# Optimization experiments

Measured on AMD Instinct MI355X. Metric: run time of the kernel, lower is better.

## Reference

```python
import jax, jax.numpy as jnp
import numpy as np
import math

B, S, D, H, HD, DC, FF, E, K = 4, 2048, 576, 9, 64, 64, 1536, 8, 2
EPS = 1e-6


def _rms(x):
    # RMSNorm with weight=ones (module instantiates a fresh RMSNorm in forward)
    return x / jnp.sqrt(jnp.mean(x * x, axis=-1, keepdims=True) + EPS)


def _expert(h, wa, wb, wc):
    return (jax.nn.gelu(h @ wa, approximate=False) * (h @ wc)) @ wb


def _forward(x, q_w, kv_w, o_w, gate_w, w1, w2, w3, sw1, sw2, sw3):
    # ---------------- MLA ----------------
    xn = _rms(x)
    q = (xn @ q_w).reshape(B, S, H, HD)
    kv = (xn @ kv_w).reshape(B, S, H, 2 * DC)
    k, v = kv[..., :DC], kv[..., DC:]
    # RoPE (complex-pair form) applied to q only, as in the source
    theta = 1.0 / (10000.0 ** (jnp.arange(0, HD, 2, dtype=jnp.float32) / HD))
    freqs = jnp.arange(S, dtype=jnp.float32)[:, None] * theta[None, :]  # [S, HD/2]
    cos = jnp.cos(freqs)[None, :, None, :]
    sin = jnp.sin(freqs)[None, :, None, :]
    qp = q.reshape(B, S, H, HD // 2, 2)
    qe, qo = qp[..., 0], qp[..., 1]
    q = jnp.stack([qe * cos - qo * sin, qe * sin + qo * cos], axis=-1).reshape(B, S, H, HD)
    # NOTE: source matmul attends head-vs-head per token: [B,S,H,HD] x [B,S,DC,H] -> [B,S,H,H]
    attn = jnp.einsum('bshd,bstd->bsht', q, k) / math.sqrt(HD)
    attn = jax.nn.softmax(attn, axis=-1)
    ao = jnp.einsum('bsht,bstd->bshd', attn, v)  # [B,S,H,DC]
    # faithful to torch: transpose(1,2).contiguous().view(B,S,D)
    ao = ao.transpose(0, 2, 1, 3).reshape(B, S, D)
    x = ao @ o_w + x
    # ---------------- MoE ----------------
    xn = _rms(x)
    gw = jax.nn.softmax(xn @ gate_w, axis=-1)  # [B,S,E]
    tw, ti = jax.lax.top_k(gw, K)
    tw = tw / jnp.sum(tw, axis=-1, keepdims=True)
    # combine weights per expert: zero for unselected experts (same math as masked loop)
    comb = jnp.sum(tw[..., None] * jax.nn.one_hot(ti, E, dtype=x.dtype), axis=-2)  # [B,S,E]
    h1 = jax.nn.gelu(jnp.einsum('bsd,edf->ebsf', xn, w1), approximate=False)
    h3 = jnp.einsum('bsd,edf->ebsf', xn, w3)
    eo = jnp.einsum('ebsf,efd->ebsd', h1 * h3, w2)  # [E,B,S,D]
    moe_out = jnp.einsum('ebsd,bse->bsd', eo, comb)
    shared = _expert(xn, sw1, sw2, sw3)
    return moe_out + shared + x


def setup_inputs() -> dict:
    key = jax.random.key(0)
    ks = jax.random.split(key, 11)
    s = 0.02
    return {
        'x': jax.random.normal(ks[0], (B, S, D), dtype=jnp.float32),
        'q_w': jax.random.normal(ks[1], (D, D), dtype=jnp.float32) * s,
        'kv_w': jax.random.normal(ks[2], (D, H * 2 * DC), dtype=jnp.float32) * s,
        'o_w': jax.random.normal(ks[3], (D, D), dtype=jnp.float32) * s,
        'gate_w': jax.random.normal(ks[4], (D, E), dtype=jnp.float32) * s,
        'w1': jax.random.normal(ks[5], (E, D, FF), dtype=jnp.float32) * s,
        'w2': jax.random.normal(ks[6], (E, FF, D), dtype=jnp.float32) * s,
        'w3': jax.random.normal(ks[7], (E, D, FF), dtype=jnp.float32) * s,
        'sw1': jax.random.normal(ks[8], (D, FF), dtype=jnp.float32) * s,
        'sw2': jax.random.normal(ks[9], (FF, D), dtype=jnp.float32) * s,
        'sw3': jax.random.normal(ks[10], (D, FF), dtype=jnp.float32) * s,
    }


def reference(x, q_w, kv_w, o_w, gate_w, w1, w2, w3, sw1, sw2, sw3):
    return _forward(x, q_w, kv_w, o_w, gate_w, w1, w2, w3, sw1, sw2, sw3)
```

## Files before the change

kernel.cpp:

```cpp
#include <hip/hip_runtime.h>
#include <math.h>

#define B_  4
#define S_  2048
#define D_  576
#define H_  9
#define HD_ 64
#define FF_ 1536
#define E_  8
#define TOK (B_*S_)
#define T1ROWS 17408

typedef unsigned int   u32x4  __attribute__((ext_vector_type(4)));
typedef unsigned short u16x8  __attribute__((ext_vector_type(8)));
typedef __bf16         bf16x8 __attribute__((ext_vector_type(8)));
typedef _Float16       f16x8  __attribute__((ext_vector_type(8)));
typedef float          f32x4  __attribute__((ext_vector_type(4)));

__device__ __forceinline__ float b2f(unsigned short u) {
    union { unsigned int i; float f; } v; v.i = ((unsigned int)u) << 16; return v.f;
}
__device__ __forceinline__ unsigned short f2b(float f) {
    unsigned int u = __builtin_bit_cast(unsigned int, f);
    unsigned int r = 0x7fffu + ((u >> 16) & 1u);
    return (unsigned short)((u + r) >> 16);
}

__global__ __launch_bounds__(256)
void rmsnorm_k(const float* __restrict__ x, unsigned short* __restrict__ xn) {
    int tok = blockIdx.x, tid = threadIdx.x;
    const float* xr = x + (size_t)tok * D_;
    float v0 = xr[tid];
    float v1 = xr[tid + 256];
    float v2 = (tid < D_ - 512) ? xr[tid + 512] : 0.f;
    float ss = v0*v0 + v1*v1 + v2*v2;
    #pragma unroll
    for (int d = 1; d < 64; d <<= 1) ss += __shfl_xor(ss, d, 64);
    __shared__ float red[4];
    if ((tid & 63) == 0) red[tid >> 6] = ss;
    __syncthreads();
    float tot = red[0] + red[1] + red[2] + red[3];
    float rms = rsqrtf(tot / (float)D_ + 1e-6f);
    unsigned short* orow = xn + (size_t)tok * D_;
    orow[tid]       = f2b(v0 * rms);
    orow[tid + 256] = f2b(v1 * rms);
    if (tid < D_ - 512) orow[tid + 512] = f2b(v2 * rms);
}

__global__ __launch_bounds__(256)
void rms32_k(const float* __restrict__ x, float* __restrict__ xn) {
    int tok = blockIdx.x, tid = threadIdx.x;
    const float* xr = x + (size_t)tok * D_;
    float v0 = xr[tid];
    float v1 = xr[tid + 256];
    float v2 = (tid < D_ - 512) ? xr[tid + 512] : 0.f;
    float ss = v0*v0 + v1*v1 + v2*v2;
    #pragma unroll
    for (int d = 1; d < 64; d <<= 1) ss += __shfl_xor(ss, d, 64);
    __shared__ float red[4];
    if ((tid & 63) == 0) red[tid >> 6] = ss;
    __syncthreads();
    float tot = red[0] + red[1] + red[2] + red[3];
    float rms = rsqrtf(tot / (float)D_ + 1e-6f);
    float* orow = xn + (size_t)tok * D_;
    orow[tid]       = v0 * rms;
    orow[tid + 256] = v1 * rms;
    if (tid < D_ - 512) orow[tid + 512] = v2 * rms;
}

__global__ __launch_bounds__(256)
void convw_k(const float* __restrict__ src, unsigned short* __restrict__ dst,
             int K, int N, long long sstr, long long dstr)
{
    __shared__ unsigned short t[64][72];
    int n0 = blockIdx.x * 64, k0 = blockIdx.y * 64;
    const float* s = src + (long long)blockIdx.z * sstr;
    unsigned short* d = dst + (long long)blockIdx.z * dstr;
    int tx = threadIdx.x & 63, ty = threadIdx.x >> 6;
    #pragma unroll
    for (int i = 0; i < 16; ++i) {
        int k = i * 4 + ty;
        t[k][tx] = f2b(s[(size_t)(k0 + k) * N + n0 + tx]);
    }
    __syncthreads();
    int r = threadIdx.x >> 3, c8 = (threadIdx.x & 7) * 8;
    #pragma unroll
    for (int it = 0; it < 2; ++it, r += 32) {
        u16x8 v;
        #pragma unroll
        for (int j = 0; j < 8; ++j) v[j] = t[c8 + j][r];
        *(u16x8*)&d[(size_t)(n0 + r) * K + k0 + c8] = v;
    }
}

__global__ __launch_bounds__(256)
void convS_k(const float* __restrict__ src,
             _Float16* __restrict__ dh, _Float16* __restrict__ dl,
             int K, int N)
{
    __shared__ _Float16 th[64][72], tl[64][72];
    int n0 = blockIdx.x * 64, k0 = blockIdx.y * 64;
    int tx = threadIdx.x & 63, ty = threadIdx.x >> 6;
    #pragma unroll
    for (int i = 0; i < 16; ++i) {
        int k = i * 4 + ty;
        float v = src[(size_t)(k0 + k) * N + n0 + tx];
        _Float16 h = (_Float16)v;
        th[k][tx] = h;
        tl[k][tx] = (_Float16)((v - (float)h) * 2048.0f);
    }
    __syncthreads();
    int r = threadIdx.x >> 3, c8 = (threadIdx.x & 7) * 8;
    #pragma unroll
    for (int it = 0; it < 2; ++it, r += 32) {
        f16x8 vh, vl;
        #pragma unroll
        for (int j = 0; j < 8; ++j) { vh[j] = th[c8 + j][r]; vl[j] = tl[c8 + j][r]; }
        *(f16x8*)&dh[(size_t)(n0 + r) * K + k0 + c8] = vh;
        *(f16x8*)&dl[(size_t)(n0 + r) * K + k0 + c8] = vl;
    }
}

template<int BN, int EPI, int WB>
__global__ __launch_bounds__(256)
void gemmS_k(const float* __restrict__ A, const float* __restrict__ Bm,
             const _Float16* __restrict__ Bhp, const _Float16* __restrict__ Blp,
             float* __restrict__ Cout, const float* __restrict__ resid,
             int M, int N, int K, int ldb)
{
    constexpr int BM = 128, BK = 64, LDT = BK + 8;
    constexpr int WM = BM / 2, WN = BN / 2, MI = WM / 16, NJ = WN / 16;
    __shared__ alignas(16) _Float16 Ah[BM][LDT], Al[BM][LDT];
    __shared__ alignas(16) _Float16 Bh[BN][LDT], Bl[BN][LDT];
    const int tid  = threadIdx.x;
    const int bn0  = blockIdx.x * BN, bm0 = blockIdx.y * BM;
    const int lane = tid & 63, wave = tid >> 6;
    const int l    = lane & 15, quad = lane >> 4;
    const int wm   = wave >> 1, wn = wave & 1;

    f32x4 accH[MI][NJ], accL[MI][NJ];
    #pragma unroll
    for (int mi = 0; mi < MI; ++mi)
        #pragma unroll
        for (int nj = 0; nj < NJ; ++nj) {
            accH[mi][nj] = (f32x4){0.f, 0.f, 0.f, 0.f};
            accL[mi][nj] = (f32x4){0.f, 0.f, 0.f, 0.f};
        }

    const int nK = K / BK;
    for (int kc = 0; kc < nK; ++kc) {
        __syncthreads();
        #pragma unroll
        for (int i = 0; i < (BM * BK) / 2048; ++i) {
            int u = i * 256 + tid;
            int r = u >> 3, c8 = (u & 7) * 8;
            const float* ga = A + (size_t)(bm0 + r) * K + kc * BK + c8;
            f16x8 hh, ll;
            #pragma unroll
            for (int j = 0; j < 8; ++j) {
                float v = ga[j];
                _Float16 h = (_Float16)v;
                hh[j] = h;
                ll[j] = (_Float16)((v - (float)h) * 2048.0f);
            }
            *(f16x8*)&Ah[r][c8] = hh;
            *(f16x8*)&Al[r][c8] = ll;
        }
        if constexpr (WB == 1) {
            #pragma unroll
            for (int i = 0; i < (BN * BK) / 2048; ++i) {
                int u = i * 256 + tid;
                int n = u >> 3, c8 = (u & 7) * 8;
                *(f16x8*)&Bh[n][c8] =
                    *(const f16x8*)(Bhp + (size_t)(bn0 + n) * K + kc * BK + c8);
                *(f16x8*)&Bl[n][c8] =
                    *(const f16x8*)(Blp + (size_t)(bn0 + n) * K + kc * BK + c8);
            }
        } else {
            #pragma unroll
            for (int i = 0; i < (BN * BK) / 2048; ++i) {
                int u = i * 256 + tid;
                int n = u % BN, k8 = (u / BN) * 8;
                const float* gB = Bm + (size_t)(kc * BK + k8) * ldb + bn0 + n;
                f16x8 hh, ll;
                #pragma unroll
                for (int j = 0; j < 8; ++j) {
                    float v = gB[(size_t)j * ldb];
                    _Float16 h = (_Float16)v;
                    hh[j] = h;
                    ll[j] = (_Float16)((v - (float)h) * 2048.0f);
                }
                *(f16x8*)&Bh[n][k8] = hh;
                *(f16x8*)&Bl[n][k8] = ll;
            }
        }
        __syncthreads();
        #pragma unroll
        for (int ks = 0; ks < BK; ks += 32) {
            f16x8 ah[MI], al[MI], bh[NJ], bl[NJ];
            #pragma unroll
            for (int mi = 0; mi < MI; ++mi) {
                ah[mi] = *(const f16x8*)&Ah[wm * WM + mi * 16 + l][ks + quad * 8];
                al[mi] = *(const f16x8*)&Al[wm * WM + mi * 16 + l][ks + quad * 8];
            }
            #pragma unroll
            for (int nj = 0; nj < NJ; ++nj) {
                bh[nj] = *(const f16x8*)&Bh[wn * WN + nj * 16 + l][ks + quad * 8];
                bl[nj] = *(const f16x8*)&Bl[wn * WN + nj * 16 + l][ks + quad * 8];
            }
            #pragma unroll
            for (int mi = 0; mi < MI; ++mi)
                #pragma unroll
                for (int nj = 0; nj < NJ; ++nj) {
                    accH[mi][nj] = __builtin_amdgcn_mfma_f32_16x16x32_f16(
                        ah[mi], bh[nj], accH[mi][nj], 0, 0, 0);
                    accL[mi][nj] = __builtin_amdgcn_mfma_f32_16x16x32_f16(
                        ah[mi], bl[nj], accL[mi][nj], 0, 0, 0);
                    accL[mi][nj] = __builtin_amdgcn_mfma_f32_16x16x32_f16(
                        al[mi], bh[nj], accL[mi][nj], 0, 0, 0);
                }
        }
    }
    #pragma unroll
    for (int mi = 0; mi < MI; ++mi)
        #pragma unroll
        for (int nj = 0; nj < NJ; ++nj)
            #pragma unroll
            for (int r = 0; r < 4; ++r) {
                int row = bm0 + wm * WM + mi * 16 + quad * 4 + r;
                int col = bn0 + wn * WN + nj * 16 + l;
                float v = accH[mi][nj][r] + accL[mi][nj][r] * (1.0f / 2048.0f);
                size_t idx = (size_t)row * N + col;
                if constexpr (EPI == 0) Cout[idx] = v;
                else                    Cout[idx] = v + resid[idx];
            }
}

template<int ROUTED>
__global__ __launch_bounds__(256, 2)
void gemm13_k(const unsigned short* __restrict__ A,
              const unsigned short* __restrict__ B1,
              const unsigned short* __restrict__ B3,
              unsigned short* __restrict__ T1o,
              const int* __restrict__ eidx,
              const int* __restrict__ counts,
              const int* __restrict__ offs,
              int M, int N, long long bstr)
{
    constexpr int BM = 128, BN = 128, BK = 64, LDT = BK + 8;
    constexpr int MI = 4, NJ = 4;
    __shared__ alignas(16) unsigned short As[BM][LDT];
    __shared__ alignas(16) unsigned short Bs1[BN][LDT];
    __shared__ alignas(16) unsigned short Bs3[BN][LDT];
    __shared__ int rowbuf[BM];
    const int tid  = threadIdx.x;
    const int bn0  = blockIdx.x * BN, bm0 = blockIdx.y * BM;
    const int lane = tid & 63, wave = tid >> 6;
    const int l    = lane & 15, quad = lane >> 4;
    const int wm   = wave >> 1, wn = wave & 1;
    const int rs   = tid >> 3, c8 = (tid & 7) * 8;

    int cnt = M, crow0 = 0;
    if constexpr (ROUTED) {
        int e = blockIdx.z;
        cnt = counts[e];
        if (bm0 >= cnt) return;
        crow0 = offs[e];
        B1 += (long long)e * bstr;
        B3 += (long long)e * bstr;
        if (tid < BM) {
            int rr = bm0 + tid;
            rowbuf[tid] = (rr < cnt) ? eidx[e * TOK + rr] : 0;
        }
        __syncthreads();
    }

    f32x4 acc1[MI][NJ], acc3[MI][NJ];
    #pragma unroll
    for (int mi = 0; mi < MI; ++mi)
        #pragma unroll
        for (int nj = 0; nj < NJ; ++nj) {
            acc1[mi][nj] = (f32x4){0.f, 0.f, 0.f, 0.f};
            acc3[mi][nj] = (f32x4){0.f, 0.f, 0.f, 0.f};
        }

    const int nK = D_ / BK;
    u32x4 ra[4], rb1[4], rb3[4];
    #pragma unroll
    for (int i = 0; i < 4; ++i) {
        int r = i * 32 + rs;
        int arow = ROUTED ? rowbuf[r] : (bm0 + r);
        ra[i]  = *(const u32x4*)(A  + (size_t)arow * D_ + c8);
        rb1[i] = *(const u32x4*)(B1 + (size_t)(bn0 + r) * D_ + c8);
        rb3[i] = *(const u32x4*)(B3 + (size_t)(bn0 + r) * D_ + c8);
    }
    for (int kc = 0; kc < nK; ++kc) {
        __syncthreads();
        #pragma unroll
        for (int i = 0; i < 4; ++i) {
            int r = i * 32 + rs;
            *(u32x4*)&As[r][c8]  = ra[i];
            *(u32x4*)&Bs1[r][c8] = rb1[i];
            *(u32x4*)&Bs3[r][c8] = rb3[i];
        }
        __syncthreads();
        if (kc + 1 < nK) {
            int ko = (kc + 1) * BK;
            #pragma unroll
            for (int i = 0; i < 4; ++i) {
                int r = i * 32 + rs;
                int arow = ROUTED ? rowbuf[r] : (bm0 + r);
                ra[i]  = *(const u32x4*)(A  + (size_t)arow * D_ + ko + c8);
                rb1[i] = *(const u32x4*)(B1 + (size_t)(bn0 + r) * D_ + ko + c8);
                rb3[i] = *(const u32x4*)(B3 + (size_t)(bn0 + r) * D_ + ko + c8);
            }
        }
        #pragma unroll
        for (int ks = 0; ks < BK; ks += 32) {
            bf16x8 af[MI], b1f[NJ], b3f[NJ];
            #pragma unroll
            for (int mi = 0; mi < MI; ++mi)
                af[mi] = __builtin_bit_cast(bf16x8,
                    *(const u32x4*)&As[wm * 64 + mi * 16 + l][ks + quad * 8]);
            #pragma unroll
            for (int nj = 0; nj < NJ; ++nj) {
                b1f[nj] = __builtin_bit_cast(bf16x8,
                    *(const u32x4*)&Bs1[wn * 64 + nj * 16 + l][ks + quad * 8]);
                b3f[nj] = __builtin_bit_cast(bf16x8,
                    *(const u32x4*)&Bs3[wn * 64 + nj * 16 + l][ks + quad * 8]);
            }
            #pragma unroll
            for (int mi = 0; mi < MI; ++mi)
                #pragma unroll
                for (int nj = 0; nj < NJ; ++nj) {
                    acc1[mi][nj] = __builtin_amdgcn_mfma_f32_16x16x32_bf16(
                        af[mi], b1f[nj], acc1[mi][nj], 0, 0, 0);
                    acc3[mi][nj] = __builtin_amdgcn_mfma_f32_16x16x32_bf16(
                        af[mi], b3f[nj], acc3[mi][nj], 0, 0, 0);
                }
        }
    }
    #pragma unroll
    for (int mi = 0; mi < MI; ++mi)
        #pragma unroll
        for (int nj = 0; nj < NJ; ++nj)
            #pragma unroll
            for (int r = 0; r < 4; ++r) {
                int lrow = bm0 + wm * 64 + mi * 16 + quad * 4 + r;
                int col  = bn0 + wn * 64 + nj * 16 + l;
                float hv = b2f(f2b(acc1[mi][nj][r]));
                float g  = 0.5f * hv * (1.0f + erff(hv * 0.70710678118654752f));
                T1o[(size_t)(crow0 + lrow) * N + col] = f2b(g * acc3[mi][nj][r]);
            }
}

template<int BN, int EPI, int ROUTED, int WB>
__global__ __launch_bounds__(256)
void gemm_k(const unsigned short* __restrict__ A,
            const void* __restrict__ Bm,
            void* __restrict__ Cout,
            const void* __restrict__ resid,
            const float* __restrict__ wgt,
            const int* __restrict__ eidx,
            const int* __restrict__ counts,
            const int* __restrict__ offs,
            int M, int N, int K, int ldb, long long bstr)
{
    constexpr int BM = 128, BK = 64, LDT = BK + 8;
    constexpr int WM = BM / 2, WN = BN / 2, MI = WM / 16, NJ = WN / 16;
    constexpr int AIT = (BM * BK) / 2048, BIT = (BN * BK) / 2048;
    __shared__ alignas(16) unsigned short As[BM][LDT];
    __shared__ alignas(16) unsigned short Bs[BN][LDT];
    __shared__ int rowbuf[BM];
    const int tid  = threadIdx.x;
    const int bn0  = blockIdx.x * BN, bm0 = blockIdx.y * BM;
    const int lane = tid & 63, wave = tid >> 6;
    const int l    = lane & 15, quad = lane >> 4;
    const int wm   = wave >> 1, wn = wave & 1;

    int cnt = M, crow0 = 0, ebase = 0;
    long long boff = 0;
    if constexpr (ROUTED) {
        int e = blockIdx.z;
        cnt = counts[e];
        if (bm0 >= cnt) return;
        crow0 = offs[e];
        ebase = e * TOK;
        boff  = (long long)e * bstr;
        if (tid < BM) {
            int rr = bm0 + tid;
            rowbuf[tid] = (rr < cnt) ? eidx[ebase + rr] : 0;
        }
        __syncthreads();
    }

    f32x4 acc[MI][NJ];
    #pragma unroll
    for (int mi = 0; mi < MI; ++mi)
        #pragma unroll
        for (int nj = 0; nj < NJ; ++nj) acc[mi][nj] = (f32x4){0.f, 0.f, 0.f, 0.f};

    const int nK = K / BK;
    u32x4 pa[AIT], pb[BIT];
    if constexpr (WB == 1) {
        const unsigned short* Bt = (const unsigned short*)Bm + boff;
        #pragma unroll
        for (int i = 0; i < AIT; ++i) {
            int r = i * 32 + (tid >> 3), c8 = (tid & 7) * 8;
            int arow;
            if constexpr (ROUTED && EPI != 5) arow = rowbuf[r];
            else if constexpr (ROUTED)        arow = crow0 + bm0 + r;
            else                              arow = bm0 + r;
            pa[i] = *(const u32x4*)(A + (size_t)arow * K + c8);
        }
        #pragma unroll
        for (int i = 0; i < BIT; ++i) {
            int n = i * 32 + (tid >> 3), c8 = (tid & 7) * 8;
            pb[i] = *(const u32x4*)(Bt + (size_t)(bn0 + n) * ldb + c8);
        }
    }
    for (int kc = 0; kc < nK; ++kc) {
        __syncthreads();
        if constexpr (WB == 1) {
            #pragma unroll
            for (int i = 0; i < AIT; ++i) {
                int r = i * 32 + (tid >> 3), c8 = (tid & 7) * 8;
                *(u32x4*)&As[r][c8] = pa[i];
            }
            #pragma unroll
            for (int i = 0; i < BIT; ++i) {
                int n = i * 32 + (tid >> 3), c8 = (tid & 7) * 8;
                *(u32x4*)&Bs[n][c8] = pb[i];
            }
        } else {
            #pragma unroll
            for (int i = 0; i < AIT; ++i) {
                int u = i * 256 + tid;
                int r = u >> 3, c8 = (u & 7) * 8;
                int arow;
                if constexpr (ROUTED && EPI != 5) arow = rowbuf[r];
                else if constexpr (ROUTED)        arow = crow0 + bm0 + r;
                else                              arow = bm0 + r;
                *(u32x4*)&As[r][c8] =
                    *(const u32x4*)(A + (size_t)arow * K + kc * BK + c8);
            }
            const float* Bf = (const float*)Bm + boff;
            #pragma unroll
            for (int i = 0; i < BIT; ++i) {
                int u = i * 256 + tid;
                int n = u % BN, k8 = (u / BN) * 8;
                const float* gB = Bf + (size_t)(kc * BK + k8) * ldb + bn0 + n;
                u16x8 tmp;
                #pragma unroll
                for (int j = 0; j < 8; ++j) tmp[j] = f2b(gB[(size_t)j * ldb]);
                *(u16x8*)&Bs[n][k8] = tmp;
            }
        }
        __syncthreads();
        if constexpr (WB == 1) {
            if (kc + 1 < nK) {
                int ko = (kc + 1) * BK;
                const unsigned short* Bt = (const unsigned short*)Bm + boff;
                #pragma unroll
                for (int i = 0; i < AIT; ++i) {
                    int r = i * 32 + (tid >> 3), c8 = (tid & 7) * 8;
                    int arow;
                    if constexpr (ROUTED && EPI != 5) arow = rowbuf[r];
                    else if constexpr (ROUTED)        arow = crow0 + bm0 + r;
                    else                              arow = bm0 + r;
                    pa[i] = *(const u32x4*)(A + (size_t)arow * K + ko + c8);
                }
                #pragma unroll
                for (int i = 0; i < BIT; ++i) {
                    int n = i * 32 + (tid >> 3), c8 = (tid & 7) * 8;
                    pb[i] = *(const u32x4*)(Bt + (size_t)(bn0 + n) * ldb + ko + c8);
                }
            }
        }
        #pragma unroll
        for (int ks = 0; ks < BK; ks += 32) {
            bf16x8 af[MI], bfr[NJ];
            #pragma unroll
            for (int mi = 0; mi < MI; ++mi)
                af[mi] = __builtin_bit_cast(bf16x8,
                    *(const u32x4*)&As[wm * WM + mi * 16 + l][ks + quad * 8]);
            #pragma unroll
            for (int nj = 0; nj < NJ; ++nj)
                bfr[nj] = __builtin_bit_cast(bf16x8,
                    *(const u32x4*)&Bs[wn * WN + nj * 16 + l][ks + quad * 8]);
            #pragma unroll
            for (int mi = 0; mi < MI; ++mi)
                #pragma unroll
                for (int nj = 0; nj < NJ; ++nj)
                    acc[mi][nj] = __builtin_amdgcn_mfma_f32_16x16x32_bf16(
                        af[mi], bfr[nj], acc[mi][nj], 0, 0, 0);
        }
    }
    #pragma unroll
    for (int mi = 0; mi < MI; ++mi)
        #pragma unroll
        for (int nj = 0; nj < NJ; ++nj)
            #pragma unroll
            for (int r = 0; r < 4; ++r) {
                int lrow = bm0 + wm * WM + mi * 16 + quad * 4 + r;
                int col  = bn0 + wn * WN + nj * 16 + l;
                float v = acc[mi][nj][r];
                if constexpr (EPI == 0) {
                    ((unsigned short*)Cout)[(size_t)(crow0 + lrow) * N + col] = f2b(v);
                } else if constexpr (EPI == 3) {
                    size_t ix = (size_t)(crow0 + lrow) * N + col;
                    float hv = b2f(((const unsigned short*)resid)[ix]);
                    float g = 0.5f * hv * (1.0f + erff(hv * 0.70710678118654752f));
                    ((unsigned short*)Cout)[ix] = f2b(g * v);
                } else if constexpr (EPI == 4) {
                    ((float*)Cout)[(size_t)lrow * N + col] += v;
                } else {
                    if (lrow < cnt) {
                        int   tok = rowbuf[lrow - bm0];
                        float sc  = wgt[ebase + lrow];
                        atomicAdd(&((float*)Cout)[(size_t)tok * N + col], sc * v);
                    }
                }
            }
}

__global__ __launch_bounds__(256)
void attn32_k(const float* __restrict__ q,
              const float* __restrict__ kv,
              float* __restrict__ ao,
              int pos0)
{
    int pl   = blockIdx.x * 4 + (threadIdx.x >> 6);
    int lane = threadIdx.x & 63;
    int pos  = pos0 + pl;
    int b = pos >> 11, s = pos & 2047;

    const float* qp  = q  + (size_t)pl * 576;
    const float* kvp = kv + (size_t)pl * 1152;

    int i = lane >> 1;
    float theta = powf(10000.f, -(float)i * (1.0f / 32.0f));
    float sn, cs;
    sincosf((float)s * theta, &sn, &cs);

    float qr[H_], kr[H_], vr[H_];
    #pragma unroll
    for (int h = 0; h < H_; ++h) {
        float qv = qp[h * 64 + lane];
        float qo = __shfl_xor(qv, 1, 64);
        qr[h] = (lane & 1) ? (qo * sn + qv * cs) : (qv * cs - qo * sn);
        kr[h] = kvp[h * 128 + lane];
        vr[h] = kvp[h * 128 + 64 + lane];
    }

    #pragma unroll
    for (int h = 0; h < H_; ++h) {
        float sc[H_];
        #pragma unroll
        for (int t = 0; t < H_; ++t) {
            float p = qr[h] * kr[t];
            #pragma unroll
            for (int d = 1; d < 64; d <<= 1) p += __shfl_xor(p, d, 64);
            sc[t] = p * 0.125f;
        }
        float mx = sc[0];
        #pragma unroll
        for (int t = 1; t < H_; ++t) mx = fmaxf(mx, sc[t]);
        float ssum = 0.f;
        #pragma unroll
        for (int t = 0; t < H_; ++t) { sc[t] = __expf(sc[t] - mx); ssum += sc[t]; }
        float inv = 1.0f / ssum;
        float ov = 0.f;
        #pragma unroll
        for (int t = 0; t < H_; ++t) ov += sc[t] * vr[t];
        ao[((size_t)(b * H_ + h) * S_ + s) * 64 + lane] = ov * inv;
    }
}

__global__ __launch_bounds__(256)
void gate1_k(const float* __restrict__ x2,
             const float* __restrict__ gw,
             float* __restrict__ tw,
             int*   __restrict__ tsel)
{
    int tok  = blockIdx.x * 4 + (threadIdx.x >> 6);
    int lane = threadIdx.x & 63;
    float acc[8];
    #pragma unroll
    for (int e = 0; e < 8; ++e) acc[e] = 0.f;
    float ss = 0.f;
    for (int d = lane; d < D_; d += 64) {
        float xv = x2[(size_t)tok * D_ + d];
        ss += xv * xv;
        const float* wr = gw + (size_t)d * 8;
        #pragma unroll
        for (int e = 0; e < 8; ++e) acc[e] += xv * wr[e];
    }
    #pragma unroll
    for (int d = 1; d < 64; d <<= 1) ss += __shfl_xor(ss, d, 64);
    #pragma unroll
    for (int e = 0; e < 8; ++e)
        #pragma unroll
        for (int d = 1; d < 64; d <<= 1) acc[e] += __shfl_xor(acc[e], d, 64);
    if (lane == 0) {
        float rms = rsqrtf(ss / (float)D_ + 1e-6f);
        #pragma unroll
        for (int e = 0; e < 8; ++e) acc[e] *= rms;
        float mx = acc[0];
        #pragma unroll
        for (int e = 1; e < 8; ++e) mx = fmaxf(mx, acc[e]);
        float g[8], ssum = 0.f;
        #pragma unroll
        for (int e = 0; e < 8; ++e) { g[e] = __expf(acc[e] - mx); ssum += g[e]; }
        #pragma unroll
        for (int e = 0; e < 8; ++e) g[e] /= ssum;
        int i1 = 0;
        #pragma unroll
        for (int e = 1; e < 8; ++e) if (g[e] > g[i1]) i1 = e;
        int i2 = -1;
        #pragma unroll
        for (int e = 0; e < 8; ++e)
            if (e != i1 && (i2 < 0 || g[e] > g[i2])) i2 = e;
        float s2 = g[i1] + g[i2];
        tw[(size_t)tok * 2 + 0] = g[i1] / s2;
        tw[(size_t)tok * 2 + 1] = g[i2] / s2;
        tsel[tok] = i1 | (i2 << 8);
    }
}

__global__ __launch_bounds__(256)
void gate2_k(const int*   __restrict__ tsel,
             const float* __restrict__ tw,
             float* __restrict__ wgt,
             int*   __restrict__ eidx,
             int*   __restrict__ counts)
{
    int e    = blockIdx.x;
    int tid  = threadIdx.x;
    int lane = tid & 63, wv = tid >> 6;
    __shared__ int wtot[4];
    int base = 0;
    for (int t0 = 0; t0 < TOK; t0 += 256) {
        int tok = t0 + tid;
        int s = tsel[tok];
        int hit = 0; float w = 0.f;
        if ((s & 255) == e)      { hit = 1; w = tw[(size_t)tok * 2 + 0]; }
        else if ((s >> 8) == e)  { hit = 1; w = tw[(size_t)tok * 2 + 1]; }
        unsigned long long m = __ballot(hit);
        int pre = __popcll(m & ((1ull << lane) - 1ull));
        if (lane == 0) wtot[wv] = __popcll(m);
        __syncthreads();
        int off = base;
        for (int q = 0; q < wv; ++q) off += wtot[q];
        if (hit) {
            int p = off + pre;
            eidx[e * TOK + p] = tok;
            wgt [e * TOK + p] = w;
        }
        base += wtot[0] + wtot[1] + wtot[2] + wtot[3];
        __syncthreads();
    }
    if (tid == 0) counts[e] = base;
}

__global__ void offs_k(const int* __restrict__ counts, int* __restrict__ offs) {
    if (threadIdx.x == 0) {
        int run = 0;
        for (int e = 0; e < 8; ++e) {
            offs[e] = run;
            run += ((counts[e] + 127) >> 7) << 7;
        }
    }
}

extern "C" void kernel_launch(void* const* d_in, const int* in_sizes, int n_in,
                              void* d_out, int out_size, void* d_ws, size_t ws_size,
                              hipStream_t stream)
{
    const float* x      = (const float*)d_in[0];
    const float* q_w    = (const float*)d_in[1];
    const float* kv_w   = (const float*)d_in[2];
    const float* o_w    = (const float*)d_in[3];
    const float* gate_w = (const float*)d_in[4];
    const float* w1     = (const float*)d_in[5];
    const float* w2     = (const float*)d_in[6];
    const float* w3     = (const float*)d_in[7];
    const float* sw1    = (const float*)d_in[8];
    const float* sw2    = (const float*)d_in[9];
    const float* sw3    = (const float*)d_in[10];
    float* out = (float*)d_out;

    const size_t XN = (size_t)TOK * D_ * 2;
    char* ws = (char*)d_ws;
    unsigned short* xn16 = (unsigned short*)ws;
    float*          ao32 = (float*)(ws + XN);

    const size_t QE = (size_t)D_ * D_, KVE = (size_t)1152 * D_;
    const size_t SW = (2 * QE + KVE) * 2 * 2;
    _Float16* qwh  = (_Float16*)(ws + 3 * XN);
    _Float16* qwl  = qwh  + QE;
    _Float16* kvwh = qwl  + QE;
    _Float16* kvwl = kvwh + KVE;
    _Float16* owh  = kvwl + KVE;
    _Float16* owl  = owh  + QE;

    bool convA = true;
    int TC = -1;
    for (int pass = 0; pass < 2; ++pass) {
        size_t base = 3 * XN + (convA ? SW : 0);
        if      (base + 8*XN    <= ws_size) { TC = 1; break; }
        else if (base + 8*XN/2  <= ws_size) { TC = 2; break; }
        else if (base + 8*XN/4  <= ws_size) { TC = 4; break; }
        else if (base + 8*XN/8  <= ws_size) { TC = 8; break; }
        else if (base + 8*XN/16 <= ws_size) { TC = 16; break; }
        else if (base + 8*XN/32 <= ws_size) { TC = 32; break; }
        else if (base + 8*XN/64 <= ws_size) { TC = 64; break; }
        convA = false;
    }
    if (TC < 0) { convA = false; TC = 64; }
    const int CT = TOK / TC;
    float* xn32c = (float*)(ws + 3*XN + (convA ? SW : 0));
    float* qc    = xn32c + (size_t)CT * D_;
    float* kvc   = qc    + (size_t)CT * D_;

    int*   counts = (int*)(ws + XN);
    int*   offs   = counts + 16;
    float* wgt    = (float*)(ws + XN + 256);
    int*   eidx   = (int*)  (ws + XN + 256 + (size_t)8 * TOK * 4);
    float* tw     = (float*)(ws + XN + 256 + (size_t)8 * TOK * 8);
    int*   tsel   = (int*)  (ws + XN + 256 + (size_t)8 * TOK * 8 + (size_t)TOK * 8);
    const size_t fixedG = XN + 256 + (size_t)8 * TOK * 8 + (size_t)TOK * 12;

    const size_t WELEM = (size_t)D_ * FF_;
    const size_t WSZ   = 27 * WELEM * 2;
    const size_t t1sz  = (size_t)T1ROWS * FF_ * 2;

    bool conv; int FC;
    if      (fixedG + WSZ + t1sz   <= ws_size) { conv = true;  FC = 1; }
    else if (fixedG + WSZ + t1sz/2 <= ws_size) { conv = true;  FC = 2; }
    else if (fixedG + WSZ + t1sz/4 <= ws_size) { conv = true;  FC = 4; }
    else if (fixedG + t1sz         <= ws_size) { conv = false; FC = 1; }
    else if (fixedG + t1sz/2       <= ws_size) { conv = false; FC = 2; }
    else                                       { conv = false; FC = 4; }
    const int FFc = FF_ / FC;

    unsigned short* wt1  = (unsigned short*)(ws + fixedG);
    unsigned short* wt3  = wt1 + 8 * WELEM;
    unsigned short* wt2  = wt3 + 8 * WELEM;
    unsigned short* swt1 = wt2 + 8 * WELEM;
    unsigned short* swt3 = swt1 + WELEM;
    unsigned short* swt2 = swt3 + WELEM;
    unsigned short* t1   = (unsigned short*)(ws + fixedG + (conv ? WSZ : 0));

    if (convA) {
        convS_k<<<dim3(D_/64,  D_/64), 256, 0, stream>>>(q_w,  qwh,  qwl,  D_, D_);
        convS_k<<<dim3(1152/64, D_/64), 256, 0, stream>>>(kv_w, kvwh, kvwl, D_, 1152);
        convS_k<<<dim3(D_/64,  D_/64), 256, 0, stream>>>(o_w,  owh,  owl,  D_, D_);
    }
    for (int t = 0; t < TC; ++t) {
        const float* xc = x + (size_t)t * CT * D_;
        rms32_k<<<CT, 256, 0, stream>>>(xc, xn32c);
        if (convA) {
            gemmS_k<64, 0, 1><<<dim3(D_ / 64, CT / 128), 256, 0, stream>>>(
                xn32c, nullptr, qwh, qwl, qc, nullptr, CT, D_, D_, D_);
            gemmS_k<64, 0, 1><<<dim3(1152 / 64, CT / 128), 256, 0, stream>>>(
                xn32c, nullptr, kvwh, kvwl, kvc, nullptr, CT, 1152, D_, D_);
        } else {
            gemmS_k<64, 0, 0><<<dim3(D_ / 64, CT / 128), 256, 0, stream>>>(
                xn32c, q_w, nullptr, nullptr, qc, nullptr, CT, D_, D_, D_);
            gemmS_k<64, 0, 0><<<dim3(1152 / 64, CT / 128), 256, 0, stream>>>(
                xn32c, kv_w, nullptr, nullptr, kvc, nullptr, CT, 1152, D_, 1152);
        }
        attn32_k<<<CT / 4, 256, 0, stream>>>(qc, kvc, ao32, t * CT);
    }
    if (convA)
        gemmS_k<64, 1, 1><<<dim3(D_ / 64, TOK / 128), 256, 0, stream>>>(
            ao32, nullptr, owh, owl, out, x, TOK, D_, D_, D_);
    else
        gemmS_k<64, 1, 0><<<dim3(D_ / 64, TOK / 128), 256, 0, stream>>>(
            ao32, o_w, nullptr, nullptr, out, x, TOK, D_, D_, D_);
    rmsnorm_k<<<TOK, 256, 0, stream>>>(out, xn16);
    gate1_k<<<TOK / 4, 256, 0, stream>>>(out, gate_w, tw, tsel);
    gate2_k<<<E_, 256, 0, stream>>>(tsel, tw, wgt, eidx, counts);
    offs_k<<<1, 64, 0, stream>>>(counts, offs);
    if (conv) {
        convw_k<<<dim3(FF_/64, D_/64, 8), 256, 0, stream>>>(
            w1, wt1, D_, FF_, (long long)D_ * FF_, (long long)FF_ * D_);
        convw_k<<<dim3(FF_/64, D_/64, 8), 256, 0, stream>>>(
            w3, wt3, D_, FF_, (long long)D_ * FF_, (long long)FF_ * D_);
        convw_k<<<dim3(D_/64, FF_/64, 8), 256, 0, stream>>>(
            w2, wt2, FF_, D_, (long long)FF_ * D_, (long long)D_ * FF_);
        convw_k<<<dim3(FF_/64, D_/64, 1), 256, 0, stream>>>(
            sw1, swt1, D_, FF_, 0, 0);
        convw_k<<<dim3(FF_/64, D_/64, 1), 256, 0, stream>>>(
            sw3, swt3, D_, FF_, 0, 0);
        convw_k<<<dim3(D_/64, FF_/64, 1), 256, 0, stream>>>(
            sw2, swt2, FF_, D_, 0, 0);
    }
    for (int c = 0; c < FC; ++c) {
        if (conv) {
            gemm13_k<1><<<dim3(FFc / 128, TOK / 128, E_), 256, 0, stream>>>(
                xn16, wt1 + (size_t)c * FFc * D_, wt3 + (size_t)c * FFc * D_,
                t1, eidx, counts, offs, TOK, FFc, (long long)FF_ * D_);
            gemm_k<192, 5, 1, 1><<<dim3(D_ / 192, TOK / 128, E_), 256, 0, stream>>>(
                t1, wt2 + (size_t)c * FFc, out, nullptr, wgt, eidx, counts, offs,
                TOK, D_, FFc, FF_, (long long)D_ * FF_);
            gemm13_k<0><<<dim3(FFc / 128, TOK / 128), 256, 0, stream>>>(
                xn16, swt1 + (size_t)c * FFc * D_, swt3 + (size_t)c * FFc * D_,
                t1, nullptr, nullptr, nullptr, TOK, FFc, 0);
            gemm_k<192, 4, 0, 1><<<dim3(D_ / 192, TOK / 128), 256, 0, stream>>>(
                t1, swt2 + (size_t)c * FFc, out, nullptr, nullptr, nullptr, nullptr, nullptr,
                TOK, D_, FFc, FF_, 0);
        } else {
            const float* w1c = w1 + (size_t)c * FFc;
            const float* w3c = w3 + (size_t)c * FFc;
            const float* w2c = w2 + (size_t)c * FFc * D_;
            gemm_k<128, 0, 1, 0><<<dim3(FFc / 128, TOK / 128, E_), 256, 0, stream>>>(
                xn16, w1c, t1, nullptr, wgt, eidx, counts, offs,
                TOK, FFc, D_, FF_, (long long)D_ * FF_);
            gemm_k<128, 3, 1, 0><<<dim3(FFc / 128, TOK / 128, E_), 256, 0, stream>>>(
                xn16, w3c, t1, t1, wgt, eidx, counts, offs,
                TOK, FFc, D_, FF_, (long long)D_ * FF_);
            gemm_k<64, 5, 1, 0><<<dim3(D_ / 64, TOK / 128, E_), 256, 0, stream>>>(
                t1, w2c, out, nullptr, wgt, eidx, counts, offs,
                TOK, D_, FFc, D_, (long long)FF_ * D_);
            gemm_k<128, 0, 0, 0><<<dim3(FFc / 128, TOK / 128), 256, 0, stream>>>(
                xn16, sw1 + (size_t)c * FFc, t1, nullptr, nullptr, nullptr, nullptr, nullptr,
                TOK, FFc, D_, FF_, 0);
            gemm_k<128, 3, 0, 0><<<dim3(FFc / 128, TOK / 128), 256, 0, stream>>>(
                xn16, sw3 + (size_t)c * FFc, t1, t1, nullptr, nullptr, nullptr, nullptr,
                TOK, FFc, D_, FF_, 0);
            gemm_k<64, 4, 0, 0><<<dim3(D_ / 64, TOK / 128), 256, 0, stream>>>(
                t1, sw2 + (size_t)c * FFc * D_, out, nullptr, nullptr, nullptr, nullptr, nullptr,
                TOK, D_, FFc, D_, 0);
        }
    }
}
```

Baseline: 704.1 us.

## Fold shared expert into routed MoE grid, swizzle LDS, merge weight conversions

The shared expert becomes a ninth 'expert' that every token routes to with weight one. Its up and down GEMMs then run inside the same routed launches as the eight experts, so two separate launches go away and the tail wave fills better. Weight conversion is merged into two launches, and the LDS tiles in the split-fp16 and bf16 GEMMs switch from padded rows to an XOR swizzle, which saves shared memory. gemm13 launch bounds rise to three blocks per SM to raise occupancy, at the cost of fewer registers per thread, and the t1 buffer grows to hold the extra rows.

```diff
diff --git a/kernel.cpp b/kernel.cpp
--- a/kernel.cpp
+++ b/kernel.cpp
@@ -10,6 +10,7 @@
 #define E_  8
 #define TOK (B_*S_)
 #define T1ROWS 17408
+#define T1ALL  25600
 
 typedef unsigned int   u32x4  __attribute__((ext_vector_type(4)));
 typedef unsigned short u16x8  __attribute__((ext_vector_type(8)));
@@ -69,13 +70,48 @@
 }
 
 __global__ __launch_bounds__(256)
-void convw_k(const float* __restrict__ src, unsigned short* __restrict__ dst,
-             int K, int N, long long sstr, long long dstr)
-{
+void convw13_k(const float* __restrict__ w1, const float* __restrict__ w3,
+               const float* __restrict__ sw1, const float* __restrict__ sw3,
+               unsigned short* __restrict__ wt1, unsigned short* __restrict__ wt3)
+{
+    const size_t WE = (size_t)D_ * FF_;
+    int z = blockIdx.z;
+    const float* s; unsigned short* d;
+    if (z < 8)       { s = w1 + (size_t)z * WE;       d = wt1 + (size_t)z * WE; }
+    else if (z == 8) { s = sw1;                        d = wt1 + 8 * WE; }
+    else if (z < 17) { s = w3 + (size_t)(z - 9) * WE;  d = wt3 + (size_t)(z - 9) * WE; }
+    else             { s = sw3;                        d = wt3 + 8 * WE; }
+    const int K = D_, N = FF_;
     __shared__ unsigned short t[64][72];
     int n0 = blockIdx.x * 64, k0 = blockIdx.y * 64;
-    const float* s = src + (long long)blockIdx.z * sstr;
-    unsigned short* d = dst + (long long)blockIdx.z * dstr;
+    int tx = threadIdx.x & 63, ty = threadIdx.x >> 6;
+    #pragma unroll
+    for (int i = 0; i < 16; ++i) {
+        int k = i * 4 + ty;
+        t[k][tx] = f2b(s[(size_t)(k0 + k) * N + n0 + tx]);
+    }
+    __syncthreads();
+    int r = threadIdx.x >> 3, c8 = (threadIdx.x & 7) * 8;
+    #pragma unroll
+    for (int it = 0; it < 2; ++it, r += 32) {
+        u16x8 v;
+        #pragma unroll
+        for (int j = 0; j < 8; ++j) v[j] = t[c8 + j][r];
+        *(u16x8*)&d[(size_t)(n0 + r) * K + k0 + c8] = v;
+    }
+}
+
+__global__ __launch_bounds__(256)
+void convw2_k(const float* __restrict__ w2, const float* __restrict__ sw2,
+              unsigned short* __restrict__ wt2)
+{
+    const size_t WE = (size_t)D_ * FF_;
+    int z = blockIdx.z;
+    const float* s = (z < 8) ? w2 + (size_t)z * WE : sw2;
+    unsigned short* d = wt2 + (size_t)z * WE;
+    const int K = FF_, N = D_;
+    __shared__ unsigned short t[64][72];
+    int n0 = blockIdx.x * 64, k0 = blockIdx.y * 64;
     int tx = threadIdx.x & 63, ty = threadIdx.x >> 6;
     #pragma unroll
     for (int i = 0; i < 16; ++i) {
@@ -128,15 +164,16 @@
              float* __restrict__ Cout, const float* __restrict__ resid,
              int M, int N, int K, int ldb)
 {
-    constexpr int BM = 128, BK = 64, LDT = BK + 8;
+    constexpr int BM = 128, BK = 64;
     constexpr int WM = BM / 2, WN = BN / 2, MI = WM / 16, NJ = WN / 16;
-    __shared__ alignas(16) _Float16 Ah[BM][LDT], Al[BM][LDT];
-    __shared__ alignas(16) _Float16 Bh[BN][LDT], Bl[BN][LDT];
+    __shared__ alignas(16) _Float16 Ah[BM][BK], Al[BM][BK];
+    __shared__ alignas(16) _Float16 Bh[BN][BK], Bl[BN][BK];
     const int tid  = threadIdx.x;
     const int bn0  = blockIdx.x * BN, bm0 = blockIdx.y * BM;
     const int lane = tid & 63, wave = tid >> 6;
     const int l    = lane & 15, quad = lane >> 4;
     const int wm   = wave >> 1, wn = wave & 1;
+    const int rsz  = (l & 7) << 3;
 
     f32x4 accH[MI][NJ], accL[MI][NJ];
     #pragma unroll
@@ -154,6 +191,7 @@
         for (int i = 0; i < (BM * BK) / 2048; ++i) {
             int u = i * 256 + tid;
             int r = u >> 3, c8 = (u & 7) * 8;
+            int cs = c8 ^ ((r & 7) << 3);
             const float* ga = A + (size_t)(bm0 + r) * K + kc * BK + c8;
             f16x8 hh, ll;
             #pragma unroll
@@ -163,17 +201,18 @@
                 hh[j] = h;
                 ll[j] = (_Float16)((v - (float)h) * 2048.0f);
             }
-            *(f16x8*)&Ah[r][c8] = hh;
-            *(f16x8*)&Al[r][c8] = ll;
+            *(f16x8*)&Ah[r][cs] = hh;
+            *(f16x8*)&Al[r][cs] = ll;
         }
         if constexpr (WB == 1) {
             #pragma unroll
             for (int i = 0; i < (BN * BK) / 2048; ++i) {
                 int u = i * 256 + tid;
                 int n = u >> 3, c8 = (u & 7) * 8;
-                *(f16x8*)&Bh[n][c8] =
+                int cs = c8 ^ ((n & 7) << 3);
+                *(f16x8*)&Bh[n][cs] =
                     *(const f16x8*)(Bhp + (size_t)(bn0 + n) * K + kc * BK + c8);
-                *(f16x8*)&Bl[n][c8] =
+                *(f16x8*)&Bl[n][cs] =
                     *(const f16x8*)(Blp + (size_t)(bn0 + n) * K + kc * BK + c8);
             }
         } else {
@@ -181,6 +220,7 @@
             for (int i = 0; i < (BN * BK) / 2048; ++i) {
                 int u = i * 256 + tid;
                 int n = u % BN, k8 = (u / BN) * 8;
+                int cs = k8 ^ ((n & 7) << 3);
                 const float* gB = Bm + (size_t)(kc * BK + k8) * ldb + bn0 + n;
                 f16x8 hh, ll;
                 #pragma unroll
@@ -190,23 +230,24 @@
                     hh[j] = h;
                     ll[j] = (_Float16)((v - (float)h) * 2048.0f);
                 }
-                *(f16x8*)&Bh[n][k8] = hh;
-                *(f16x8*)&Bl[n][k8] = ll;
+                *(f16x8*)&Bh[n][cs] = hh;
+                *(f16x8*)&Bl[n][cs] = ll;
             }
         }
         __syncthreads();
         #pragma unroll
         for (int ks = 0; ks < BK; ks += 32) {
             f16x8 ah[MI], al[MI], bh[NJ], bl[NJ];
+            int col = (ks + quad * 8) ^ rsz;
             #pragma unroll
             for (int mi = 0; mi < MI; ++mi) {
-                ah[mi] = *(const f16x8*)&Ah[wm * WM + mi * 16 + l][ks + quad * 8];
-                al[mi] = *(const f16x8*)&Al[wm * WM + mi * 16 + l][ks + quad * 8];
+                ah[mi] = *(const f16x8*)&Ah[wm * WM + mi * 16 + l][col];
+                al[mi] = *(const f16x8*)&Al[wm * WM + mi * 16 + l][col];
             }
             #pragma unroll
             for (int nj = 0; nj < NJ; ++nj) {
-                bh[nj] = *(const f16x8*)&Bh[wn * WN + nj * 16 + l][ks + quad * 8];
-                bl[nj] = *(const f16x8*)&Bl[wn * WN + nj * 16 + l][ks + quad * 8];
+                bh[nj] = *(const f16x8*)&Bh[wn * WN + nj * 16 + l][col];
+                bl[nj] = *(const f16x8*)&Bl[wn * WN + nj * 16 + l][col];
             }
             #pragma unroll
             for (int mi = 0; mi < MI; ++mi)
@@ -236,8 +277,7 @@
             }
 }
 
-template<int ROUTED>
-__global__ __launch_bounds__(256, 2)
+__global__ __launch_bounds__(256, 3)
 void gemm13_k(const unsigned short* __restrict__ A,
               const unsigned short* __restrict__ B1,
               const unsigned short* __restrict__ B3,
@@ -245,35 +285,34 @@
               const int* __restrict__ eidx,
               const int* __restrict__ counts,
               const int* __restrict__ offs,
-              int M, int N, long long bstr)
-{
-    constexpr int BM = 128, BN = 128, BK = 64, LDT = BK + 8;
+              int N, long long bstr)
+{
+    constexpr int BM = 128, BK = 64;
     constexpr int MI = 4, NJ = 4;
-    __shared__ alignas(16) unsigned short As[BM][LDT];
-    __shared__ alignas(16) unsigned short Bs1[BN][LDT];
-    __shared__ alignas(16) unsigned short Bs3[BN][LDT];
+    __shared__ alignas(16) unsigned short As[BM][BK];
+    __shared__ alignas(16) unsigned short Bs1[BM][BK];
+    __shared__ alignas(16) unsigned short Bs3[BM][BK];
     __shared__ int rowbuf[BM];
     const int tid  = threadIdx.x;
-    const int bn0  = blockIdx.x * BN, bm0 = blockIdx.y * BM;
+    const int bn0  = blockIdx.x * 128, bm0 = blockIdx.y * 128;
     const int lane = tid & 63, wave = tid >> 6;
     const int l    = lane & 15, quad = lane >> 4;
     const int wm   = wave >> 1, wn = wave & 1;
     const int rs   = tid >> 3, c8 = (tid & 7) * 8;
-
-    int cnt = M, crow0 = 0;
-    if constexpr (ROUTED) {
-        int e = blockIdx.z;
-        cnt = counts[e];
-        if (bm0 >= cnt) return;
-        crow0 = offs[e];
-        B1 += (long long)e * bstr;
-        B3 += (long long)e * bstr;
-        if (tid < BM) {
-            int rr = bm0 + tid;
-            rowbuf[tid] = (rr < cnt) ? eidx[e * TOK + rr] : 0;
-        }
-        __syncthreads();
-    }
+    const int wsz  = (rs & 7) << 3;
+    const int rsz  = (l & 7) << 3;
+
+    int e = blockIdx.z;
+    int cnt = counts[e];
+    if (bm0 >= cnt) return;
+    int crow0 = offs[e];
+    B1 += (long long)e * bstr;
+    B3 += (long long)e * bstr;
+    if (tid < BM) {
+        int rr = bm0 + tid;
+        rowbuf[tid] = (rr < cnt) ? eidx[e * TOK + rr] : 0;
+    }
+    __syncthreads();
 
     f32x4 acc1[MI][NJ], acc3[MI][NJ];
     #pragma unroll
@@ -289,7 +328,7 @@
     #pragma unroll
     for (int i = 0; i < 4; ++i) {
         int r = i * 32 + rs;
-        int arow = ROUTED ? rowbuf[r] : (bm0 + r);
+        int arow = rowbuf[r];
         ra[i]  = *(const u32x4*)(A  + (size_t)arow * D_ + c8);
         rb1[i] = *(const u32x4*)(B1 + (size_t)(bn0 + r) * D_ + c8);
         rb3[i] = *(const u32x4*)(B3 + (size_t)(bn0 + r) * D_ + c8);
@@ -299,9 +338,9 @@
         #pragma unroll
         for (int i = 0; i < 4; ++i) {
             int r = i * 32 + rs;
-            *(u32x4*)&As[r][c8]  = ra[i];
-            *(u32x4*)&Bs1[r][c8] = rb1[i];
-            *(u32x4*)&Bs3[r][c8] = rb3[i];
+            *(u32x4*)&As[r][c8 ^ wsz]  = ra[i];
+            *(u32x4*)&Bs1[r][c8 ^ wsz] = rb1[i];
+            *(u32x4*)&Bs3[r][c8 ^ wsz] = rb3[i];
         }
         __syncthreads();
         if (kc + 1 < nK) {
@@ -309,7 +348,7 @@
             #pragma unroll
             for (int i = 0; i < 4; ++i) {
                 int r = i * 32 + rs;
-                int arow = ROUTED ? rowbuf[r] : (bm0 + r);
+                int arow = rowbuf[r];
                 ra[i]  = *(const u32x4*)(A  + (size_t)arow * D_ + ko + c8);
                 rb1[i] = *(const u32x4*)(B1 + (size_t)(bn0 + r) * D_ + ko + c8);
                 rb3[i] = *(const u32x4*)(B3 + (size_t)(bn0 + r) * D_ + ko + c8);
@@ -318,16 +357,17 @@
         #pragma unroll
         for (int ks = 0; ks < BK; ks += 32) {
             bf16x8 af[MI], b1f[NJ], b3f[NJ];
+            int col = (ks + quad * 8) ^ rsz;
             #pragma unroll
             for (int mi = 0; mi < MI; ++mi)
                 af[mi] = __builtin_bit_cast(bf16x8,
-                    *(const u32x4*)&As[wm * 64 + mi * 16 + l][ks + quad * 8]);
+                    *(const u32x4*)&As[wm * 64 + mi * 16 + l][col]);
             #pragma unroll
             for (int nj = 0; nj < NJ; ++nj) {
                 b1f[nj] = __builtin_bit_cast(bf16x8,
-                    *(const u32x4*)&Bs1[wn * 64 + nj * 16 + l][ks + quad * 8]);
+                    *(const u32x4*)&Bs1[wn * 64 + nj * 16 + l][col]);
                 b3f[nj] = __builtin_bit_cast(bf16x8,
-                    *(const u32x4*)&Bs3[wn * 64 + nj * 16 + l][ks + quad * 8]);
+                    *(const u32x4*)&Bs3[wn * 64 + nj * 16 + l][col]);
             }
             #pragma unroll
             for (int mi = 0; mi < MI; ++mi)
@@ -642,10 +682,13 @@
     int base = 0;
     for (int t0 = 0; t0 < TOK; t0 += 256) {
         int tok = t0 + tid;
-        int s = tsel[tok];
         int hit = 0; float w = 0.f;
-        if ((s & 255) == e)      { hit = 1; w = tw[(size_t)tok * 2 + 0]; }
-        else if ((s >> 8) == e)  { hit = 1; w = tw[(size_t)tok * 2 + 1]; }
+        if (e == E_) { hit = 1; w = 1.0f; }
+        else {
+            int s = tsel[tok];
+            if ((s & 255) == e)      { hit = 1; w = tw[(size_t)tok * 2 + 0]; }
+            else if ((s >> 8) == e)  { hit = 1; w = tw[(size_t)tok * 2 + 1]; }
+        }
         unsigned long long m = __ballot(hit);
         int pre = __popcll(m & ((1ull << lane) - 1ull));
         if (lane == 0) wtot[wv] = __popcll(m);
@@ -666,7 +709,7 @@
 __global__ void offs_k(const int* __restrict__ counts, int* __restrict__ offs) {
     if (threadIdx.x == 0) {
         int run = 0;
-        for (int e = 0; e < 8; ++e) {
+        for (int e = 0; e < 9; ++e) {
             offs[e] = run;
             run += ((counts[e] + 127) >> 7) << 7;
         }
@@ -726,31 +769,27 @@
     int*   counts = (int*)(ws + XN);
     int*   offs   = counts + 16;
     float* wgt    = (float*)(ws + XN + 256);
-    int*   eidx   = (int*)  (ws + XN + 256 + (size_t)8 * TOK * 4);
-    float* tw     = (float*)(ws + XN + 256 + (size_t)8 * TOK * 8);
-    int*   tsel   = (int*)  (ws + XN + 256 + (size_t)8 * TOK * 8 + (size_t)TOK * 8);
-    const size_t fixedG = XN + 256 + (size_t)8 * TOK * 8 + (size_t)TOK * 12;
+    int*   eidx   = (int*)  (ws + XN + 256 + (size_t)9 * TOK * 4);
+    float* tw     = (float*)(ws + XN + 256 + (size_t)9 * TOK * 8);
+    int*   tsel   = (int*)  (ws + XN + 256 + (size_t)9 * TOK * 8 + (size_t)TOK * 8);
+    const size_t fixedG = XN + 256 + (size_t)9 * TOK * 8 + (size_t)TOK * 12;
 
     const size_t WELEM = (size_t)D_ * FF_;
     const size_t WSZ   = 27 * WELEM * 2;
-    const size_t t1sz  = (size_t)T1ROWS * FF_ * 2;
 
     bool conv; int FC;
-    if      (fixedG + WSZ + t1sz   <= ws_size) { conv = true;  FC = 1; }
-    else if (fixedG + WSZ + t1sz/2 <= ws_size) { conv = true;  FC = 2; }
-    else if (fixedG + WSZ + t1sz/4 <= ws_size) { conv = true;  FC = 4; }
-    else if (fixedG + t1sz         <= ws_size) { conv = false; FC = 1; }
-    else if (fixedG + t1sz/2       <= ws_size) { conv = false; FC = 2; }
-    else                                       { conv = false; FC = 4; }
+    if      (fixedG + WSZ + (size_t)T1ALL * FF_     * 2 <= ws_size) { conv = true;  FC = 1; }
+    else if (fixedG + WSZ + (size_t)T1ALL * (FF_/2) * 2 <= ws_size) { conv = true;  FC = 2; }
+    else if (fixedG + WSZ + (size_t)T1ALL * (FF_/4) * 2 <= ws_size) { conv = true;  FC = 4; }
+    else if (fixedG + (size_t)T1ROWS * FF_     * 2 <= ws_size)      { conv = false; FC = 1; }
+    else if (fixedG + (size_t)T1ROWS * (FF_/2) * 2 <= ws_size)      { conv = false; FC = 2; }
+    else                                                            { conv = false; FC = 4; }
     const int FFc = FF_ / FC;
 
-    unsigned short* wt1  = (unsigned short*)(ws + fixedG);
-    unsigned short* wt3  = wt1 + 8 * WELEM;
-    unsigned short* wt2  = wt3 + 8 * WELEM;
-    unsigned short* swt1 = wt2 + 8 * WELEM;
-    unsigned short* swt3 = swt1 + WELEM;
-    unsigned short* swt2 = swt3 + WELEM;
-    unsigned short* t1   = (unsigned short*)(ws + fixedG + (conv ? WSZ : 0));
+    unsigned short* wt1 = (unsigned short*)(ws + fixedG);
+    unsigned short* wt3 = wt1 + 9 * WELEM;
+    unsigned short* wt2 = wt3 + 9 * WELEM;
+    unsigned short* t1  = (unsigned short*)(ws + fixedG + (conv ? WSZ : 0));
 
     if (convA) {
         convS_k<<<dim3(D_/64,  D_/64), 256, 0, stream>>>(q_w,  qwh,  qwl,  D_, D_);
@@ -781,36 +820,21 @@
             ao32, o_w, nullptr, nullptr, out, x, TOK, D_, D_, D_);
     rmsnorm_k<<<TOK, 256, 0, stream>>>(out, xn16);
     gate1_k<<<TOK / 4, 256, 0, stream>>>(out, gate_w, tw, tsel);
-    gate2_k<<<E_, 256, 0, stream>>>(tsel, tw, wgt, eidx, counts);
+    gate2_k<<<E_ + 1, 256, 0, stream>>>(tsel, tw, wgt, eidx, counts);
     offs_k<<<1, 64, 0, stream>>>(counts, offs);
     if (conv) {
-        convw_k<<<dim3(FF_/64, D_/64, 8), 256, 0, stream>>>(
-            w1, wt1, D_, FF_, (long long)D_ * FF_, (long long)FF_ * D_);
-        convw_k<<<dim3(FF_/64, D_/64, 8), 256, 0, stream>>>(
-            w3, wt3, D_, FF_, (long long)D_ * FF_, (long long)FF_ * D_);
-        convw_k<<<dim3(D_/64, FF_/64, 8), 256, 0, stream>>>(
-            w2, wt2, FF_, D_, (long long)FF_ * D_, (long long)D_ * FF_);
-        convw_k<<<dim3(FF_/64, D_/64, 1), 256, 0, stream>>>(
-            sw1, swt1, D_, FF_, 0, 0);
-        convw_k<<<dim3(FF_/64, D_/64, 1), 256, 0, stream>>>(
-            sw3, swt3, D_, FF_, 0, 0);
-        convw_k<<<dim3(D_/64, FF_/64, 1), 256, 0, stream>>>(
-            sw2, swt2, FF_, D_, 0, 0);
+        convw13_k<<<dim3(FF_/64, D_/64, 18), 256, 0, stream>>>(
+            w1, w3, sw1, sw3, wt1, wt3);
+        convw2_k<<<dim3(D_/64, FF_/64, 9), 256, 0, stream>>>(w2, sw2, wt2);
     }
     for (int c = 0; c < FC; ++c) {
         if (conv) {
-            gemm13_k<1><<<dim3(FFc / 128, TOK / 128, E_), 256, 0, stream>>>(
+            gemm13_k<<<dim3(FFc / 128, TOK / 128, 9), 256, 0, stream>>>(
                 xn16, wt1 + (size_t)c * FFc * D_, wt3 + (size_t)c * FFc * D_,
-                t1, eidx, counts, offs, TOK, FFc, (long long)FF_ * D_);
-            gemm_k<192, 5, 1, 1><<<dim3(D_ / 192, TOK / 128, E_), 256, 0, stream>>>(
+                t1, eidx, counts, offs, FFc, (long long)WELEM);
+            gemm_k<192, 5, 1, 1><<<dim3(D_ / 192, TOK / 128, 9), 256, 0, stream>>>(
                 t1, wt2 + (size_t)c * FFc, out, nullptr, wgt, eidx, counts, offs,
-                TOK, D_, FFc, FF_, (long long)D_ * FF_);
-            gemm13_k<0><<<dim3(FFc / 128, TOK / 128), 256, 0, stream>>>(
-                xn16, swt1 + (size_t)c * FFc * D_, swt3 + (size_t)c * FFc * D_,
-                t1, nullptr, nullptr, nullptr, TOK, FFc, 0);
-            gemm_k<192, 4, 0, 1><<<dim3(D_ / 192, TOK / 128), 256, 0, stream>>>(
-                t1, swt2 + (size_t)c * FFc, out, nullptr, nullptr, nullptr, nullptr, nullptr,
-                TOK, D_, FFc, FF_, 0);
+                TOK, D_, FFc, FF_, (long long)WELEM);
         } else {
             const float* w1c = w1 + (size_t)c * FFc;
             const float* w3c = w3 + (size_t)c * FFc;
```

New measurement: 882.9 us. 1.25x slower.
